# Kernel optimization log

Hardware: AMD Instinct MI355X
Metric: run time of the kernel (lower is better)

The kernel has to match this reference:

```python
import jax, jax.numpy as jnp
import numpy as np

N_VOXELS = 150000
N_PAIRS = 60000   # rulebook pairs per kernel offset
K = 27            # 3x3x3 kernel offsets
CIN, COUT = 32, 64
BN_EPS = 1e-5


def setup_inputs() -> dict:
    key = jax.random.key(0)
    ks = jax.random.split(key, 5)
    features = jax.random.normal(ks[0], (N_VOXELS, CIN), dtype=jnp.float32)
    in_idx = jax.random.randint(ks[1], (K, N_PAIRS), 0, N_VOXELS, dtype=jnp.int32)
    out_idx = jax.random.randint(ks[2], (K, N_PAIRS), 0, N_VOXELS, dtype=jnp.int32)
    # Kaiming-ish init for conv weight [K, cin, cout]
    weight = jax.random.normal(ks[3], (K, CIN, COUT), dtype=jnp.float32) * (2.0 / (K * CIN)) ** 0.5
    bias = jax.random.normal(ks[4], (COUT,), dtype=jnp.float32) * 0.01
    gamma = jnp.ones((COUT,), dtype=jnp.float32)
    beta = jnp.zeros((COUT,), dtype=jnp.float32)
    return {"features": features, "in_idx": in_idx, "out_idx": out_idx,
            "weight": weight, "bias": bias, "gamma": gamma, "beta": beta}


def reference(features, in_idx, out_idx, weight, bias, gamma, beta):
    # --- sparse conv: rulebook gather-matmul-scatter ---
    gathered = features[in_idx]                           # [K, P, cin]
    contrib = jnp.einsum('kpc,kco->kpo', gathered, weight)  # [K, P, cout]
    out = jax.ops.segment_sum(contrib.reshape(-1, COUT),
                              out_idx.reshape(-1),
                              num_segments=N_VOXELS)       # [N, cout]
    out = out + bias
    # --- ReLU (note: module applies ReLU BEFORE BatchNorm1d) ---
    out = jax.nn.relu(out)
    # --- BatchNorm1d over active voxels (training-mode batch stats) ---
    mean = jnp.mean(out, axis=0)
    var = jnp.var(out, axis=0)
    out = (out - mean) * jax.lax.rsqrt(var + BN_EPS) * gamma + beta
    return out
```

## Files before the change

### kernel.cpp

```cpp
#include <hip/hip_runtime.h>

#define N_VOXELS 150000
#define NP 60000
#define NK 27
#define CIN 32
#define COUT 64
#define BN_EPS 1e-5f
#define NELEM (N_VOXELS * COUT)

__global__ __launch_bounds__(256, 6) void conv_scatter(
    const float* __restrict__ features,
    const int* __restrict__ in_idx,
    const int* __restrict__ out_idx,
    const float* __restrict__ weight,
    float* __restrict__ accum)
{
    const int k    = blockIdx.y;
    const int lane = threadIdx.x & 63;
    const int wid  = threadIdx.x >> 6;
    const int gw   = blockIdx.x * 4 + wid;
    const int nw   = gridDim.x * 4;

    float w[CIN];
    const float* wk = weight + (size_t)k * (CIN * COUT) + lane;
#pragma unroll
    for (int c = 0; c < CIN; ++c) w[c] = wk[c * COUT];

    const int* ii = in_idx  + k * NP;
    const int* oi = out_idx + k * NP;

    for (int p = gw; p < NP; p += nw) {
        const int vin  = ii[p];
        const int vout = oi[p];
        const float4* f4p = reinterpret_cast<const float4*>(features + (size_t)vin * CIN);
        float s0 = 0.f, s1 = 0.f, s2 = 0.f, s3 = 0.f;
#pragma unroll
        for (int q = 0; q < CIN / 4; ++q) {
            float4 v = f4p[q];
            s0 = fmaf(v.x, w[4 * q + 0], s0);
            s1 = fmaf(v.y, w[4 * q + 1], s1);
            s2 = fmaf(v.z, w[4 * q + 2], s2);
            s3 = fmaf(v.w, w[4 * q + 3], s3);
        }
        atomicAdd(&accum[(size_t)vout * COUT + lane], (s0 + s1) + (s2 + s3));
    }
}

__global__ __launch_bounds__(256) void bias_relu_stats(
    const float* __restrict__ buf,
    const float* __restrict__ bias,
    float* __restrict__ stats)
{
    const int tid    = blockIdx.x * 256 + threadIdx.x;
    const int stride = gridDim.x * 256;
    const int c      = threadIdx.x & 63;
    const float b    = bias[c];

    float sum = 0.f, sumsq = 0.f;
    for (int i = tid; i < NELEM; i += stride) {
        float y = buf[i] + b;
        y = fmaxf(y, 0.f);
        sum += y;
        sumsq += y * y;
    }

    __shared__ float ls[256];
    __shared__ float lq[256];
    ls[threadIdx.x] = sum;
    lq[threadIdx.x] = sumsq;
    __syncthreads();
    if (threadIdx.x < 64) {
        float s = ls[threadIdx.x] + ls[threadIdx.x + 64] +
                  ls[threadIdx.x + 128] + ls[threadIdx.x + 192];
        float q = lq[threadIdx.x] + lq[threadIdx.x + 64] +
                  lq[threadIdx.x + 128] + lq[threadIdx.x + 192];
        atomicAdd(&stats[c], s);
        atomicAdd(&stats[64 + c], q);
    }
}

__global__ __launch_bounds__(256) void bn_apply(
    float* __restrict__ buf,
    const float* __restrict__ bias,
    const float* __restrict__ stats,
    const float* __restrict__ gamma,
    const float* __restrict__ beta)
{
    const int c = threadIdx.x & 63;
    const float inv_n = 1.f / (float)N_VOXELS;
    const float mean  = stats[c] * inv_n;
    const float var   = stats[64 + c] * inv_n - mean * mean;
    const float scale = gamma[c] * rsqrtf(var + BN_EPS);
    const float shift = beta[c] - mean * scale;
    const float b     = bias[c];

    const int tid    = blockIdx.x * 256 + threadIdx.x;
    const int stride = gridDim.x * 256;
    for (int i = tid; i < NELEM; i += stride) {
        float y = fmaxf(buf[i] + b, 0.f);
        buf[i] = fmaf(y, scale, shift);
    }
}

extern "C" void kernel_launch(void* const* d_in, const int* in_sizes, int n_in,
                              void* d_out, int out_size, void* d_ws, size_t ws_size,
                              hipStream_t stream) {
    const float* features = (const float*)d_in[0];
    const int*   in_idx   = (const int*)d_in[1];
    const int*   out_idx  = (const int*)d_in[2];
    const float* weight   = (const float*)d_in[3];
    const float* bias     = (const float*)d_in[4];
    const float* gamma    = (const float*)d_in[5];
    const float* beta     = (const float*)d_in[6];
    float* out   = (float*)d_out;
    float* stats = (float*)d_ws;

    hipMemsetAsync(d_out, 0, (size_t)out_size * sizeof(float), stream);
    hipMemsetAsync(d_ws, 0, 128 * sizeof(float), stream);

    dim3 cgrid(76, NK);
    conv_scatter<<<cgrid, 256, 0, stream>>>(features, in_idx, out_idx, weight, out);

    bias_relu_stats<<<256, 256, 0, stream>>>(out, bias, stats);

    bn_apply<<<2048, 256, 0, stream>>>(out, bias, stats, gamma, beta);
}
```

Baseline: 748.3 us.

## Bucket rulebook pairs by output region and accumulate in shared memory

Adds a pass that sorts rulebook pairs into per-64-voxel output buckets. Each block then gathers and multiplies its bucket's pairs, grouped by kernel offset, and accumulates into LDS instead of issuing global float atomics per output element. Bias, ReLU and the BN sum/sum-of-squares are fused into the write-out of that gather kernel, which also removes the output memset and one full pass over the output. bn_apply is vectorised to float4 with per-lane scale/shift. The trade-offs are an extra bucketing kernel with global atomics, a fixed per-bucket capacity of 1024 that silently drops overflow pairs, and a larger workspace requirement.

```diff
diff --git a/kernel.cpp b/kernel.cpp
--- a/kernel.cpp
+++ b/kernel.cpp
@@ -8,97 +8,143 @@
 #define BN_EPS 1e-5f
 #define NELEM (N_VOXELS * COUT)
 
-__global__ __launch_bounds__(256, 6) void conv_scatter(
+#define RVOX 64
+#define NR ((N_VOXELS + RVOX - 1) / RVOX)
+#define CAP 1024
+
+#define WS_CNT   0
+#define WS_STATS 4096
+#define WS_LIST  8192
+
+__global__ __launch_bounds__(256) void build_buckets(
+    const int* __restrict__ out_idx, int* __restrict__ ws)
+{
+    const int k = blockIdx.y;
+    const int p = blockIdx.x * 256 + threadIdx.x;
+    if (p >= NP) return;
+    const int v = out_idx[k * NP + p];
+    const int r = v >> 6;
+    const int slot = atomicAdd(&ws[WS_CNT + r], 1);
+    if (slot < CAP)
+        ws[WS_LIST + r * CAP + slot] = (k << 22) | (p << 6) | (v & 63);
+}
+
+__global__ __launch_bounds__(256) void conv_gather(
     const float* __restrict__ features,
     const int* __restrict__ in_idx,
-    const int* __restrict__ out_idx,
     const float* __restrict__ weight,
-    float* __restrict__ accum)
-{
-    const int k    = blockIdx.y;
-    const int lane = threadIdx.x & 63;
-    const int wid  = threadIdx.x >> 6;
-    const int gw   = blockIdx.x * 4 + wid;
-    const int nw   = gridDim.x * 4;
-
-    float w[CIN];
-    const float* wk = weight + (size_t)k * (CIN * COUT) + lane;
-#pragma unroll
-    for (int c = 0; c < CIN; ++c) w[c] = wk[c * COUT];
-
-    const int* ii = in_idx  + k * NP;
-    const int* oi = out_idx + k * NP;
-
-    for (int p = gw; p < NP; p += nw) {
-        const int vin  = ii[p];
-        const int vout = oi[p];
-        const float4* f4p = reinterpret_cast<const float4*>(features + (size_t)vin * CIN);
-        float s0 = 0.f, s1 = 0.f, s2 = 0.f, s3 = 0.f;
-#pragma unroll
-        for (int q = 0; q < CIN / 4; ++q) {
-            float4 v = f4p[q];
-            s0 = fmaf(v.x, w[4 * q + 0], s0);
-            s1 = fmaf(v.y, w[4 * q + 1], s1);
-            s2 = fmaf(v.z, w[4 * q + 2], s2);
-            s3 = fmaf(v.w, w[4 * q + 3], s3);
-        }
-        atomicAdd(&accum[(size_t)vout * COUT + lane], (s0 + s1) + (s2 + s3));
-    }
-}
-
-__global__ __launch_bounds__(256) void bias_relu_stats(
-    const float* __restrict__ buf,
     const float* __restrict__ bias,
+    const int* __restrict__ ws_i,
+    float* __restrict__ out,
     float* __restrict__ stats)
 {
-    const int tid    = blockIdx.x * 256 + threadIdx.x;
-    const int stride = gridDim.x * 256;
-    const int c      = threadIdx.x & 63;
-    const float b    = bias[c];
+    __shared__ float accum[RVOX * COUT];
+    __shared__ int   kbin[CAP];
+    __shared__ int   khist[NK];
+    __shared__ int   koff[NK + 1];
+    __shared__ int   kcur[NK];
+    __shared__ float lsum[COUT];
+    __shared__ float lsq[COUT];
 
-    float sum = 0.f, sumsq = 0.f;
-    for (int i = tid; i < NELEM; i += stride) {
-        float y = buf[i] + b;
+    const int r    = blockIdx.x;
+    const int tid  = threadIdx.x;
+    const int lane = tid & 63;
+    const int wid  = tid >> 6;
+
+    int n = ws_i[WS_CNT + r];
+    if (n > CAP) n = CAP;
+    const int* list = ws_i + WS_LIST + (size_t)r * CAP;
+
+    for (int i = tid; i < RVOX * COUT; i += 256) accum[i] = 0.f;
+    if (tid < NK) khist[tid] = 0;
+    if (tid < COUT) { lsum[tid] = 0.f; lsq[tid] = 0.f; }
+    __syncthreads();
+
+    for (int i = tid; i < n; i += 256) atomicAdd(&khist[list[i] >> 22], 1);
+    __syncthreads();
+    if (tid == 0) {
+        int acc = 0;
+        for (int k = 0; k < NK; ++k) { koff[k] = acc; kcur[k] = acc; acc += khist[k]; }
+        koff[NK] = acc;
+    }
+    __syncthreads();
+    for (int i = tid; i < n; i += 256) {
+        const int pk = list[i];
+        const int slot = atomicAdd(&kcur[pk >> 22], 1);
+        kbin[slot] = pk;
+    }
+    __syncthreads();
+
+    for (int k = 0; k < NK; ++k) {
+        const int b0 = koff[k], b1 = koff[k + 1];
+        if (b0 == b1) continue;
+        float w[CIN];
+        const float* wk = weight + k * (CIN * COUT) + lane;
+#pragma unroll
+        for (int c = 0; c < CIN; ++c) w[c] = wk[c * COUT];
+
+        for (int i = b0 + wid; i < b1; i += 4) {
+            const int pk  = kbin[i];
+            const int p   = (pk >> 6) & 0xFFFF;
+            const int lv  = pk & 63;
+            const int vin = in_idx[k * NP + p];
+            const float4* f4 = reinterpret_cast<const float4*>(features + (size_t)vin * CIN);
+            float s0 = 0.f, s1 = 0.f, s2 = 0.f, s3 = 0.f;
+#pragma unroll
+            for (int q = 0; q < CIN / 4; ++q) {
+                const float4 v = f4[q];
+                s0 = fmaf(v.x, w[4 * q + 0], s0);
+                s1 = fmaf(v.y, w[4 * q + 1], s1);
+                s2 = fmaf(v.z, w[4 * q + 2], s2);
+                s3 = fmaf(v.w, w[4 * q + 3], s3);
+            }
+            atomicAdd(&accum[lv * COUT + lane], (s0 + s1) + (s2 + s3));
+        }
+    }
+    __syncthreads();
+
+    const int v0 = r * RVOX;
+    const int nv = (N_VOXELS - v0 < RVOX) ? (N_VOXELS - v0) : RVOX;
+    const float b = bias[lane];
+    for (int i = tid; i < nv * COUT; i += 256) {
+        float y = accum[i] + b;
         y = fmaxf(y, 0.f);
-        sum += y;
-        sumsq += y * y;
+        out[(size_t)v0 * COUT + i] = y;
+        atomicAdd(&lsum[lane], y);
+        atomicAdd(&lsq[lane], y * y);
     }
-
-    __shared__ float ls[256];
-    __shared__ float lq[256];
-    ls[threadIdx.x] = sum;
-    lq[threadIdx.x] = sumsq;
     __syncthreads();
-    if (threadIdx.x < 64) {
-        float s = ls[threadIdx.x] + ls[threadIdx.x + 64] +
-                  ls[threadIdx.x + 128] + ls[threadIdx.x + 192];
-        float q = lq[threadIdx.x] + lq[threadIdx.x + 64] +
-                  lq[threadIdx.x + 128] + lq[threadIdx.x + 192];
-        atomicAdd(&stats[c], s);
-        atomicAdd(&stats[64 + c], q);
-    }
+    if (tid < COUT) atomicAdd(&stats[tid], lsum[tid]);
+    else if (tid < 2 * COUT) atomicAdd(&stats[tid], lsq[tid - COUT]);
 }
 
 __global__ __launch_bounds__(256) void bn_apply(
     float* __restrict__ buf,
-    const float* __restrict__ bias,
     const float* __restrict__ stats,
     const float* __restrict__ gamma,
     const float* __restrict__ beta)
 {
-    const int c = threadIdx.x & 63;
     const float inv_n = 1.f / (float)N_VOXELS;
-    const float mean  = stats[c] * inv_n;
-    const float var   = stats[64 + c] * inv_n - mean * mean;
-    const float scale = gamma[c] * rsqrtf(var + BN_EPS);
-    const float shift = beta[c] - mean * scale;
-    const float b     = bias[c];
-
+    const int cg = (threadIdx.x & 15) * 4;
+    float sc[4], sh[4];
+#pragma unroll
+    for (int j = 0; j < 4; ++j) {
+        const int c = cg + j;
+        const float mean = stats[c] * inv_n;
+        const float var  = stats[COUT + c] * inv_n - mean * mean;
+        sc[j] = gamma[c] * rsqrtf(var + BN_EPS);
+        sh[j] = beta[c] - mean * sc[j];
+    }
     const int tid    = blockIdx.x * 256 + threadIdx.x;
     const int stride = gridDim.x * 256;
-    for (int i = tid; i < NELEM; i += stride) {
-        float y = fmaxf(buf[i] + b, 0.f);
-        buf[i] = fmaf(y, scale, shift);
+    float4* buf4 = reinterpret_cast<float4*>(buf);
+    for (int i = tid; i < NELEM / 4; i += stride) {
+        float4 y = buf4[i];
+        y.x = fmaf(y.x, sc[0], sh[0]);
+        y.y = fmaf(y.y, sc[1], sh[1]);
+        y.z = fmaf(y.z, sc[2], sh[2]);
+        y.w = fmaf(y.w, sc[3], sh[3]);
+        buf4[i] = y;
     }
 }
 
@@ -113,15 +159,15 @@
     const float* gamma    = (const float*)d_in[5];
     const float* beta     = (const float*)d_in[6];
     float* out   = (float*)d_out;
-    float* stats = (float*)d_ws;
+    int*   ws    = (int*)d_ws;
+    float* stats = (float*)d_ws + WS_STATS;
 
-    hipMemsetAsync(d_out, 0, (size_t)out_size * sizeof(float), stream);
-    hipMemsetAsync(d_ws, 0, 128 * sizeof(float), stream);
+    hipMemsetAsync(d_ws, 0, (size_t)WS_LIST * sizeof(int), stream);
 
-    dim3 cgrid(76, NK);
-    conv_scatter<<<cgrid, 256, 0, stream>>>(features, in_idx, out_idx, weight, out);
+    dim3 bgrid((NP + 255) / 256, NK);
+    build_buckets<<<bgrid, 256, 0, stream>>>(out_idx, ws);
 
-    bias_relu_stats<<<256, 256, 0, stream>>>(out, bias, stats);
+    conv_gather<<<NR, 256, 0, stream>>>(features, in_idx, weight, bias, ws, out, stats);
 
-    bn_apply<<<2048, 256, 0, stream>>>(out, bias, stats, gamma, beta);
+    bn_apply<<<2048, 256, 0, stream>>>(out, stats, gamma, beta);
 }
```

Result: slower. 994.0 us (+32.8%).
